# Kernel optimization log

Hardware: AMD Instinct MI355X
Metric: run time of the kernel (lower is better)

Reference implementation:

```python
import jax, jax.numpy as jnp
import numpy as np

DIM = 1024
HEADS = 16
HEAD_DIM = DIM // HEADS
SCALE = DIM ** (-0.5)  # note: module scales by full dim, not head_dim


def setup_inputs() -> dict:
    key = jax.random.key(0)
    k1, k2, k3, k4 = jax.random.split(key, 4)
    B, N = 4, 2048
    x = jax.random.normal(k1, (B, N, DIM), dtype=jnp.float32)
    # nn.Linear(dim, 3*dim, bias=False): weight [3*dim, dim]
    w_qkv = jax.random.normal(k2, (3 * DIM, DIM), dtype=jnp.float32) * (DIM ** -0.5)
    # nn.Linear(dim, dim) with bias
    w_out = jax.random.normal(k3, (DIM, DIM), dtype=jnp.float32) * (DIM ** -0.5)
    b_out = jax.random.normal(k4, (DIM,), dtype=jnp.float32) * 0.01
    return {"x": x, "w_qkv": w_qkv, "w_out": w_out, "b_out": b_out}


def reference(x, w_qkv, w_out, b_out):
    b, n, _ = x.shape
    qkv = jnp.einsum('bnd,ed->bne', x, w_qkv)  # [b, n, 3*dim]
    # rearrange 'b n (qkv h d) -> qkv b h n d'
    qkv = qkv.reshape(b, n, 3, HEADS, HEAD_DIM)
    q, k, v = (qkv[:, :, i].transpose(0, 2, 1, 3) for i in range(3))  # [b, h, n, d]
    dots = jnp.einsum('bhid,bhjd->bhij', q, k) * SCALE
    attn = jax.nn.softmax(dots, axis=-1)
    out = jnp.einsum('bhij,bhjd->bhid', attn, v)
    out = out.transpose(0, 2, 1, 3).reshape(b, n, HEADS * HEAD_DIM)  # [b, n, dim]
    return jnp.einsum('bnd,ed->bne', out, w_out) + b_out
```

## Files before the change

### kernel.cpp

```cpp
#include <hip/hip_runtime.h>

typedef __bf16 bf16_t;
typedef __bf16 bf16x2 __attribute__((ext_vector_type(2)));
typedef __bf16 bf16x4 __attribute__((ext_vector_type(4)));
typedef __bf16 bf16x8 __attribute__((ext_vector_type(8)));
typedef float floatx4 __attribute__((ext_vector_type(4)));

__device__ __forceinline__ void gll16(const void* g, void* l) {
  __builtin_amdgcn_global_load_lds(
      (const __attribute__((address_space(1))) void*)g,
      (__attribute__((address_space(3))) void*)l, 16, 0, 0);
}

__device__ __forceinline__ bf16x8 cvt8(const float4 a, const float4 b) {
  bf16x8 v;
  v[0] = (bf16_t)a.x; v[1] = (bf16_t)a.y; v[2] = (bf16_t)a.z; v[3] = (bf16_t)a.w;
  v[4] = (bf16_t)b.x; v[5] = (bf16_t)b.y; v[6] = (bf16_t)b.z; v[7] = (bf16_t)b.w;
  return v;
}

__global__ __launch_bounds__(256)
void cvt_all(const float* __restrict__ x,  bf16_t* __restrict__ xb,
             const float* __restrict__ wq, bf16_t* __restrict__ wqb,
             const float* __restrict__ wo, bf16_t* __restrict__ wob)
{
  const int bid = blockIdx.x;
  const float* s;
  bf16_t* d;
  int i;
  if (bid < 4096)      { s = x;  d = xb;  i = bid * 256 + threadIdx.x; }
  else if (bid < 5632) { s = wq; d = wqb; i = (bid - 4096) * 256 + threadIdx.x; }
  else                 { s = wo; d = wob; i = (bid - 5632) * 256 + threadIdx.x; }
  const float4 a = ((const float4*)s)[2 * i];
  const float4 b = ((const float4*)s)[2 * i + 1];
  *(bf16x8*)(d + (size_t)i * 8) = cvt8(a, b);
}

template<bool C32>
__global__ __launch_bounds__(256, 3)
void gemm_bt(const bf16_t* __restrict__ Ab, const bf16_t* __restrict__ Wb,
             const float* __restrict__ bias, void* __restrict__ Cv,
             int M, int Nf, int K, int lda, int qcols, float qscale)
{
  __shared__ __align__(16) bf16_t lA[3][128 * 32];
  __shared__ __align__(16) bf16_t lB[3][128 * 32];

  const int tid  = threadIdx.x;
  const int wave = tid >> 6;
  const int lane = tid & 63;
  const int q    = lane >> 4;
  const int ln   = lane & 15;
  const int wm   = wave >> 1, wn = wave & 1;

  const int x     = blockIdx.x & 7;
  const int local = blockIdx.x >> 3;
  const int mt = x * 8 + (local & 7);
  const int nt = local >> 3;
  const int m0 = mt << 7, n0 = nt << 7;

  const int kiters = K >> 5;

  auto stage = [&](int buf, int k0s) {
#pragma unroll
    for (int tt = 0; tt < 2; ++tt) {
      const int rbase = tt * 64 + wave * 16;
      const int r  = rbase + (lane >> 2);
      const int gc = (lane & 3) ^ ((r >> 1) & 3);
      gll16(Ab + (size_t)(m0 + r) * lda + k0s + gc * 8, lA[buf] + rbase * 32);
      gll16(Wb + (size_t)(n0 + r) * K   + k0s + gc * 8, lB[buf] + rbase * 32);
    }
  };

  floatx4 acc[4][4] = {};

  stage(0, 0);
  stage(1, 32);

  for (int t = 0; t < kiters; ++t) {
    const int buf = t % 3;

    if (t + 1 < kiters) {
      asm volatile("s_waitcnt vmcnt(4)" ::: "memory");
    } else {
      asm volatile("s_waitcnt vmcnt(0)" ::: "memory");
    }
    __builtin_amdgcn_sched_barrier(0);
    __builtin_amdgcn_s_barrier();
    __builtin_amdgcn_sched_barrier(0);

    bf16x8 af[4], bfr[4];
#pragma unroll
    for (int i = 0; i < 4; ++i) {
      const int r = wm * 64 + i * 16 + ln;
      af[i] = *(const bf16x8*)(lA[buf] + r * 32 + (q ^ ((r >> 1) & 3)) * 8);
    }
#pragma unroll
    for (int j = 0; j < 4; ++j) {
      const int r = wn * 64 + j * 16 + ln;
      bfr[j] = *(const bf16x8*)(lB[buf] + r * 32 + (q ^ ((r >> 1) & 3)) * 8);
    }
    __builtin_amdgcn_s_setprio(1);
#pragma unroll
    for (int i = 0; i < 4; ++i)
#pragma unroll
      for (int j = 0; j < 4; ++j)
        acc[i][j] = __builtin_amdgcn_mfma_f32_16x16x32_bf16(af[i], bfr[j], acc[i][j], 0, 0, 0);
    __builtin_amdgcn_s_setprio(0);

    if (t + 2 < kiters) stage((t + 2) % 3, (t + 2) << 5);
  }

#pragma unroll
  for (int j = 0; j < 4; ++j) {
    const int col = n0 + wn * 64 + j * 16 + ln;
    const float bv = bias ? bias[col] : 0.0f;
    const float sc = (col < qcols) ? qscale : 1.0f;
#pragma unroll
    for (int i = 0; i < 4; ++i) {
      const int row = m0 + wm * 64 + i * 16 + q * 4;
#pragma unroll
      for (int r = 0; r < 4; ++r) {
        const float val = acc[i][j][r] * sc + bv;
        if constexpr (C32)
          ((float*)Cv)[(size_t)(row + r) * Nf + col] = val;
        else
          ((bf16_t*)Cv)[(size_t)(row + r) * Nf + col] = (bf16_t)val;
      }
    }
  }
}

__global__ __launch_bounds__(256, 2)
void attn_kernel(bf16_t* __restrict__ qkv)
{
  __shared__ __align__(16) bf16_t lK[2][128 * 64];
  __shared__ __align__(16) bf16_t lVT[64 * 128];
  __shared__ __align__(16) bf16_t lP[128 * 128];

  const int tid  = threadIdx.x;
  const int wave = tid >> 6;
  const int lane = tid & 63;
  const int q  = lane >> 4;
  const int ln = lane & 15;
  const int wm = wave >> 1, wn = wave & 1;

  const int hw = blockIdx.x;
  const int w  = (hw & 7) * 128 + (hw >> 3);
  const int qt = w & 15;
  const int h  = (w >> 4) & 15;
  const int b  = w >> 8;

  bf16_t* Qbase = qkv + (size_t)(b * 2048 + qt * 128) * 3072 + h * 64;
  const bf16_t* Kbase = qkv + (size_t)(b * 2048) * 3072 + 1024 + h * 64;
  const bf16_t* Vbase = qkv + (size_t)(b * 2048) * 3072 + 2048 + h * 64;

#pragma unroll
  for (int t = 0; t < 4; ++t) {
    const int rbase = t * 32 + wave * 8;
    const int r  = rbase + (lane >> 3);
    const int gc = (lane & 7) ^ (r & 7);
    gll16(Qbase + (size_t)r * 3072 + gc * 8, lP + rbase * 64);
    gll16(Kbase + (size_t)r * 3072 + gc * 8, lK[0] + rbase * 64);
  }
  __syncthreads();

  bf16x8 qf[4][2];
#pragma unroll
  for (int i = 0; i < 4; ++i) {
    const int r = wm * 64 + i * 16 + ln;
#pragma unroll
    for (int kt = 0; kt < 2; ++kt) {
      const int c = (kt * 4 + q) ^ (r & 7);
      qf[i][kt] = *(const bf16x8*)(lP + r * 64 + c * 8);
    }
  }

  bf16x8 vcur[2][2], vnxt[2][2];
#pragma unroll
  for (int it = 0; it < 2; ++it) {
    const bf16_t* src = Vbase + (size_t)(2 * lane) * 3072 + (wave + it * 4) * 8;
    vcur[it][0] = *(const bf16x8*)src;
    vcur[it][1] = *(const bf16x8*)(src + 3072);
  }

  floatx4 accO[2][4] = {};
  floatx4 accS[2] = {};

  bf16x8 ones;
#pragma unroll
  for (int j = 0; j < 8; ++j) ones[j] = (bf16_t)1.0f;

  for (int jt = 0; jt < 16; ++jt) {
    const bf16_t* lKc = lK[jt & 1];
    bf16_t*       lKn = lK[(jt & 1) ^ 1];

    __syncthreads();

#pragma unroll
    for (int it = 0; it < 2; ++it) {
      const int c = wave + it * 4;
#pragma unroll
      for (int j = 0; j < 8; ++j) {
        const int d  = c * 8 + j;
        const int ch = (lane >> 2) ^ (d & 7);
        bf16x2 pr;
        pr[0] = vcur[it][0][j];
        pr[1] = vcur[it][1][j];
        *(bf16x2*)(lVT + d * 128 + ch * 8 + ((2 * lane) & 7)) = pr;
      }
    }

    bf16x8 kf[4][2];
#pragma unroll
    for (int n = 0; n < 4; ++n) {
      const int r = wn * 64 + n * 16 + ln;
#pragma unroll
      for (int kt = 0; kt < 2; ++kt) {
        const int c = (kt * 4 + q) ^ (r & 7);
        kf[n][kt] = *(const bf16x8*)(lKc + r * 64 + c * 8);
      }
    }

    if (jt < 15) {
      const int j0n = (jt + 1) * 128;
#pragma unroll
      for (int t = 0; t < 4; ++t) {
        const int rbase = t * 32 + wave * 8;
        const int r  = rbase + (lane >> 3);
        const int gc = (lane & 7) ^ (r & 7);
        gll16(Kbase + (size_t)(j0n + r) * 3072 + gc * 8, lKn + rbase * 64);
      }
#pragma unroll
      for (int it = 0; it < 2; ++it) {
        const bf16_t* src = Vbase + (size_t)(j0n + 2 * lane) * 3072 + (wave + it * 4) * 8;
        vnxt[it][0] = *(const bf16x8*)src;
        vnxt[it][1] = *(const bf16x8*)(src + 3072);
      }
    }

    __builtin_amdgcn_s_setprio(1);
#pragma unroll
    for (int i = 0; i < 4; ++i) {
#pragma unroll
      for (int n = 0; n < 4; ++n) {
        floatx4 st = {0.0f, 0.0f, 0.0f, 0.0f};
        st = __builtin_amdgcn_mfma_f32_16x16x32_bf16(kf[i][0], qf[n][0], st, 0, 0, 0);
        st = __builtin_amdgcn_mfma_f32_16x16x32_bf16(kf[i][1], qf[n][1], st, 0, 0, 0);
        bf16x4 pk;
#pragma unroll
        for (int r = 0; r < 4; ++r)
          pk[r] = (bf16_t)__builtin_amdgcn_exp2f(st[r]);
        const int m    = wm * 64 + n * 16 + ln;
        const int tok0 = wn * 64 + i * 16 + q * 4;
        *(bf16x4*)(lP + m * 128 + (((tok0 >> 3) ^ (m & 7)) << 3) + (tok0 & 7)) = pk;
      }
    }
    __builtin_amdgcn_s_setprio(0);

    __syncthreads();

    __builtin_amdgcn_s_setprio(1);
#pragma unroll
    for (int ks = 0; ks < 4; ++ks) {
      bf16x8 bv[4];
#pragma unroll
      for (int n = 0; n < 4; ++n) {
        const int d  = n * 16 + ln;
        const int cc = (ks * 4 + q) ^ (d & 7);
        bv[n] = *(const bf16x8*)(lVT + d * 128 + cc * 8);
      }
#pragma unroll
      for (int i = 0; i < 2; ++i) {
        const int m = wave * 32 + i * 16 + ln;
        const bf16x8 ap = *(const bf16x8*)(lP + m * 128 + (((ks * 4 + q) ^ (m & 7)) << 3));
#pragma unroll
        for (int n = 0; n < 4; ++n)
          accO[i][n] = __builtin_amdgcn_mfma_f32_16x16x32_bf16(ap, bv[n], accO[i][n], 0, 0, 0);
        accS[i] = __builtin_amdgcn_mfma_f32_16x16x32_bf16(ap, ones, accS[i], 0, 0, 0);
      }
    }
    __builtin_amdgcn_s_setprio(0);

    if (jt < 15) {
#pragma unroll
      for (int it = 0; it < 2; ++it) {
        vcur[it][0] = vnxt[it][0];
        vcur[it][1] = vnxt[it][1];
      }
    }
  }

#pragma unroll
  for (int i = 0; i < 2; ++i) {
#pragma unroll
    for (int r = 0; r < 4; ++r) {
      const int row = wave * 32 + i * 16 + q * 4 + r;
      const float rcp = 1.0f / fmaxf(accS[i][r], 1e-20f);
#pragma unroll
      for (int n = 0; n < 4; ++n) {
        const int col = n * 16 + ln;
        Qbase[(size_t)row * 3072 + col] = (bf16_t)(accO[i][n][r] * rcp);
      }
    }
  }
}

extern "C" void kernel_launch(void* const* d_in, const int* in_sizes, int n_in,
                              void* d_out, int out_size, void* d_ws, size_t ws_size,
                              hipStream_t stream)
{
  const float* x     = (const float*)d_in[0];
  const float* w_qkv = (const float*)d_in[1];
  const float* w_out = (const float*)d_in[2];
  const float* b_out = (const float*)d_in[3];
  float* out = (float*)d_out;

  bf16_t* qkv    = (bf16_t*)d_ws;
  bf16_t* xb     = qkv    + (size_t)8192 * 3072;
  bf16_t* wqkvb  = xb     + (size_t)8192 * 1024;
  bf16_t* woutb  = wqkvb  + (size_t)3072 * 1024;

  const float qs = 0.04508422f;

  cvt_all<<<dim3(6144), dim3(256), 0, stream>>>(x, xb, w_qkv, wqkvb, w_out, woutb);

  gemm_bt<false><<<dim3(64 * 24), dim3(256), 0, stream>>>(
      xb, wqkvb, nullptr, qkv, 8192, 3072, 1024, 1024, 1024, qs);
  attn_kernel<<<dim3(1024), dim3(256), 0, stream>>>(qkv);
  gemm_bt<true><<<dim3(64 * 8), dim3(256), 0, stream>>>(
      qkv, woutb, b_out, out, 8192, 1024, 1024, 3072, 0, 1.0f);
}
```

Before: 262.6 us.

## Keep attention probabilities in registers and split PV across waves with final reduction

The P matrix is no longer staged through shared memory. K rows are loaded in a permuted order so the S-tile MFMA output lands in the register layout needed as the A operand of the PV MFMA. Each wave pair splits the key dimension, accumulates partial O and row sums, and combines them through an LDS reduction at the end. This removes the 32KB lP buffer and its LDS write/read traffic per tile, which may improve occupancy. In exchange it doubles the accumulator registers and adds a final reduction step.

```diff
diff --git a/kernel.cpp b/kernel.cpp
--- a/kernel.cpp
+++ b/kernel.cpp
@@ -17,6 +17,11 @@
   v[0] = (bf16_t)a.x; v[1] = (bf16_t)a.y; v[2] = (bf16_t)a.z; v[3] = (bf16_t)a.w;
   v[4] = (bf16_t)b.x; v[5] = (bf16_t)b.y; v[6] = (bf16_t)b.z; v[7] = (bf16_t)b.w;
   return v;
+}
+
+__device__ __forceinline__ int permk(int r) {
+  const int u = r & 31;
+  return (r & ~31) + (((u >> 2) & 3) << 3) + ((u >> 4) << 2) + (u & 3);
 }
 
 __global__ __launch_bounds__(256)
@@ -135,7 +140,6 @@
 {
   __shared__ __align__(16) bf16_t lK[2][128 * 64];
   __shared__ __align__(16) bf16_t lVT[64 * 128];
-  __shared__ __align__(16) bf16_t lP[128 * 128];
 
   const int tid  = threadIdx.x;
   const int wave = tid >> 6;
@@ -159,8 +163,8 @@
     const int rbase = t * 32 + wave * 8;
     const int r  = rbase + (lane >> 3);
     const int gc = (lane & 7) ^ (r & 7);
-    gll16(Qbase + (size_t)r * 3072 + gc * 8, lP + rbase * 64);
-    gll16(Kbase + (size_t)r * 3072 + gc * 8, lK[0] + rbase * 64);
+    gll16(Qbase + (size_t)r * 3072 + gc * 8, lVT + rbase * 64);
+    gll16(Kbase + (size_t)permk(r) * 3072 + gc * 8, lK[0] + rbase * 64);
   }
   __syncthreads();
 
@@ -171,7 +175,7 @@
 #pragma unroll
     for (int kt = 0; kt < 2; ++kt) {
       const int c = (kt * 4 + q) ^ (r & 7);
-      qf[i][kt] = *(const bf16x8*)(lP + r * 64 + c * 8);
+      qf[i][kt] = *(const bf16x8*)(lVT + r * 64 + c * 8);
     }
   }
 
@@ -183,8 +187,8 @@
     vcur[it][1] = *(const bf16x8*)(src + 3072);
   }
 
-  floatx4 accO[2][4] = {};
-  floatx4 accS[2] = {};
+  floatx4 accO[4][4] = {};
+  floatx4 accS[4] = {};
 
   bf16x8 ones;
 #pragma unroll
@@ -210,17 +214,6 @@
       }
     }
 
-    bf16x8 kf[4][2];
-#pragma unroll
-    for (int n = 0; n < 4; ++n) {
-      const int r = wn * 64 + n * 16 + ln;
-#pragma unroll
-      for (int kt = 0; kt < 2; ++kt) {
-        const int c = (kt * 4 + q) ^ (r & 7);
-        kf[n][kt] = *(const bf16x8*)(lKc + r * 64 + c * 8);
-      }
-    }
-
     if (jt < 15) {
       const int j0n = (jt + 1) * 128;
 #pragma unroll
@@ -228,7 +221,7 @@
         const int rbase = t * 32 + wave * 8;
         const int r  = rbase + (lane >> 3);
         const int gc = (lane & 7) ^ (r & 7);
-        gll16(Kbase + (size_t)(j0n + r) * 3072 + gc * 8, lKn + rbase * 64);
+        gll16(Kbase + (size_t)(j0n + permk(r)) * 3072 + gc * 8, lKn + rbase * 64);
       }
 #pragma unroll
       for (int it = 0; it < 2; ++it) {
@@ -238,45 +231,46 @@
       }
     }
 
+    bf16x8 ap[2][4];
     __builtin_amdgcn_s_setprio(1);
 #pragma unroll
-    for (int i = 0; i < 4; ++i) {
+    for (int c = 0; c < 2; ++c) {
+#pragma unroll
+      for (int e = 0; e < 2; ++e) {
+        const int rb = wn * 64 + (c * 2 + e) * 16 + ln;
+        const bf16x8 kf0 = *(const bf16x8*)(lKc + rb * 64 + ((q)     ^ (rb & 7)) * 8);
+        const bf16x8 kf1 = *(const bf16x8*)(lKc + rb * 64 + ((4 + q) ^ (rb & 7)) * 8);
+#pragma unroll
+        for (int n = 0; n < 4; ++n) {
+          floatx4 st = {0.0f, 0.0f, 0.0f, 0.0f};
+          st = __builtin_amdgcn_mfma_f32_16x16x32_bf16(kf0, qf[n][0], st, 0, 0, 0);
+          st = __builtin_amdgcn_mfma_f32_16x16x32_bf16(kf1, qf[n][1], st, 0, 0, 0);
+#pragma unroll
+          for (int r4 = 0; r4 < 4; ++r4)
+            ap[c][n][e * 4 + r4] = (bf16_t)__builtin_amdgcn_exp2f(st[r4]);
+        }
+      }
+    }
+    __builtin_amdgcn_s_setprio(0);
+
+    __syncthreads();
+
+    __builtin_amdgcn_s_setprio(1);
+#pragma unroll
+    for (int c = 0; c < 2; ++c) {
+      bf16x8 bv[4];
+#pragma unroll
+      for (int nd = 0; nd < 4; ++nd) {
+        const int d  = nd * 16 + ln;
+        const int cc = (wn * 8 + c * 4 + q) ^ (d & 7);
+        bv[nd] = *(const bf16x8*)(lVT + d * 128 + cc * 8);
+      }
 #pragma unroll
       for (int n = 0; n < 4; ++n) {
-        floatx4 st = {0.0f, 0.0f, 0.0f, 0.0f};
-        st = __builtin_amdgcn_mfma_f32_16x16x32_bf16(kf[i][0], qf[n][0], st, 0, 0, 0);
-        st = __builtin_amdgcn_mfma_f32_16x16x32_bf16(kf[i][1], qf[n][1], st, 0, 0, 0);
-        bf16x4 pk;
-#pragma unroll
-        for (int r = 0; r < 4; ++r)
-          pk[r] = (bf16_t)__builtin_amdgcn_exp2f(st[r]);
-        const int m    = wm * 64 + n * 16 + ln;
-        const int tok0 = wn * 64 + i * 16 + q * 4;
-        *(bf16x4*)(lP + m * 128 + (((tok0 >> 3) ^ (m & 7)) << 3) + (tok0 & 7)) = pk;
-      }
-    }
-    __builtin_amdgcn_s_setprio(0);
-
-    __syncthreads();
-
-    __builtin_amdgcn_s_setprio(1);
-#pragma unroll
-    for (int ks = 0; ks < 4; ++ks) {
-      bf16x8 bv[4];
-#pragma unroll
-      for (int n = 0; n < 4; ++n) {
-        const int d  = n * 16 + ln;
-        const int cc = (ks * 4 + q) ^ (d & 7);
-        bv[n] = *(const bf16x8*)(lVT + d * 128 + cc * 8);
-      }
-#pragma unroll
-      for (int i = 0; i < 2; ++i) {
-        const int m = wave * 32 + i * 16 + ln;
-        const bf16x8 ap = *(const bf16x8*)(lP + m * 128 + (((ks * 4 + q) ^ (m & 7)) << 3));
-#pragma unroll
-        for (int n = 0; n < 4; ++n)
-          accO[i][n] = __builtin_amdgcn_mfma_f32_16x16x32_bf16(ap, bv[n], accO[i][n], 0, 0, 0);
-        accS[i] = __builtin_amdgcn_mfma_f32_16x16x32_bf16(ap, ones, accS[i], 0, 0, 0);
+#pragma unroll
+        for (int nd = 0; nd < 4; ++nd)
+          accO[n][nd] = __builtin_amdgcn_mfma_f32_16x16x32_bf16(ap[c][n], bv[nd], accO[n][nd], 0, 0, 0);
+        accS[n] = __builtin_amdgcn_mfma_f32_16x16x32_bf16(ap[c][n], ones, accS[n], 0, 0, 0);
       }
     }
     __builtin_amdgcn_s_setprio(0);
@@ -290,16 +284,40 @@
     }
   }
 
-#pragma unroll
-  for (int i = 0; i < 2; ++i) {
-#pragma unroll
-    for (int r = 0; r < 4; ++r) {
-      const int row = wave * 32 + i * 16 + q * 4 + r;
-      const float rcp = 1.0f / fmaxf(accS[i][r], 1e-20f);
-#pragma unroll
-      for (int n = 0; n < 4; ++n) {
-        const int col = n * 16 + ln;
-        Qbase[(size_t)row * 3072 + col] = (bf16_t)(accO[i][n][r] * rcp);
+  float* red  = (float*)lK;
+  float* redS = (float*)lVT;
+
+  if (wn == 1) {
+#pragma unroll
+    for (int n = 0; n < 4; ++n)
+#pragma unroll
+      for (int nd = 0; nd < 4; ++nd)
+#pragma unroll
+        for (int r4 = 0; r4 < 4; ++r4)
+          red[wm * 4096 + (n * 16 + q * 4 + r4) * 64 + nd * 16 + ln] = accO[n][nd][r4];
+  }
+  __syncthreads();
+  if (wn == 1 && ln == 0) {
+#pragma unroll
+    for (int n = 0; n < 4; ++n)
+#pragma unroll
+      for (int r4 = 0; r4 < 4; ++r4)
+        redS[wm * 64 + n * 16 + q * 4 + r4] = accS[n][r4];
+  }
+  __syncthreads();
+  if (wn == 0) {
+#pragma unroll
+    for (int n = 0; n < 4; ++n) {
+#pragma unroll
+      for (int r4 = 0; r4 < 4; ++r4) {
+        const int m = n * 16 + q * 4 + r4;
+        const float s = accS[n][r4] + redS[wm * 64 + m];
+        const float rcp = 1.0f / fmaxf(s, 1e-20f);
+#pragma unroll
+        for (int nd = 0; nd < 4; ++nd) {
+          const float o = accO[n][nd][r4] + red[wm * 4096 + m * 64 + nd * 16 + ln];
+          Qbase[(size_t)(wm * 64 + m) * 3072 + nd * 16 + ln] = (bf16_t)(o * rcp);
+        }
       }
     }
   }
```

Measured after the change: 259.0 us. About the same (-1.4%).
